# Performance work log

Hardware: AMD Instinct MI355X
Metric: run time of the kernel (lower is better)

## Reference

```python
import jax, jax.numpy as jnp
import numpy as np

H = 16
LN_EPS = 1e-5


def setup_inputs() -> dict:
    key = jax.random.key(0)
    ks = jax.random.split(key, 8)
    B, N, D = 2, 2048, 1024
    s = D ** -0.5
    return {
        "q_s": jax.random.normal(ks[0], (B, N, D), jnp.float32),
        "pos_emb": jax.random.normal(ks[1], (B, N, D), jnp.float32),
        "Wq": jax.random.normal(ks[2], (D, D), jnp.float32) * s,
        "Wk": jax.random.normal(ks[3], (D, D), jnp.float32) * s,
        "Wv": jax.random.normal(ks[4], (D, D), jnp.float32) * s,
        "Wo": jax.random.normal(ks[5], (D, D), jnp.float32) * s,
        "bo": jnp.zeros((D,), jnp.float32),
        "ln_g": jnp.ones((D,), jnp.float32),
        "ln_b": jnp.zeros((D,), jnp.float32),
    }


def _split_heads(t):
    b, n, d = t.shape
    return t.reshape(b, n, H, d // H).transpose(0, 2, 1, 3)  # b h n d


def reference(q_s, pos_emb, Wq, Wk, Wv, Wo, bo, ln_g, ln_b):
    # self-attention: k_s = v_s = q_s
    q = _split_heads(q_s @ Wq)
    k = _split_heads(q_s @ Wk)
    v = _split_heads(q_s @ Wv)
    p = _split_heads(pos_emb)
    scale = q.shape[-1] ** -0.5
    # content-content + content-position attention logits: [b,h,i,j]
    att = (jnp.einsum('bhid,bhjd->bhij', q, k) + jnp.einsum('bhid,bhjd->bhij', q, p)) * scale
    att = jax.nn.softmax(att, axis=-1)
    o = jnp.einsum('bhij,bhjd->bhid', att, v)
    b, h, n, d = o.shape
    o = o.transpose(0, 2, 1, 3).reshape(b, n, h * d)
    o = o @ Wo + bo  # out_layer (dropout rate 0 -> identity)
    x = o + q_s  # residual
    mu = jnp.mean(x, axis=-1, keepdims=True)
    var = jnp.var(x, axis=-1, keepdims=True)
    return (x - mu) * jax.lax.rsqrt(var + LN_EPS) * ln_g + ln_b
```

## Files before the change

kernel.cpp:

```cpp
#include <hip/hip_runtime.h>
#include <hip/hip_bf16.h>
#include <stdint.h>

typedef unsigned short u16;
typedef unsigned int u32;
typedef short s16x8 __attribute__((ext_vector_type(8)));
typedef short s16x4 __attribute__((ext_vector_type(4)));
typedef float f32x4 __attribute__((ext_vector_type(4)));

#define MFMA(a, b, c) __builtin_amdgcn_mfma_f32_16x16x32_bf16((a), (b), (c), 0, 0, 0)

__device__ __forceinline__ u16 f2bf_rte(float f) {
  __hip_bfloat16 h = __float2bfloat16(f);
  u16 u;
  __builtin_memcpy(&u, &h, 2);
  return u;
}

__device__ __forceinline__ void gload16(const u16* g, u16* l) {
  __builtin_amdgcn_global_load_lds((const __attribute__((address_space(1))) u32*)g,
                                   (__attribute__((address_space(3))) u32*)l, 16, 0, 0);
}

__global__ __launch_bounds__(256) void k_cvt(const float* __restrict__ in,
                                             u16* __restrict__ out, int n8) {
  int i = blockIdx.x * 256 + threadIdx.x;
  if (i >= n8) return;
  const f32x4* p = (const f32x4*)(in + (size_t)i * 8);
  f32x4 a = p[0], b = p[1];
  s16x8 o;
  for (int k = 0; k < 4; ++k) o[k] = (short)f2bf_rte(a[k]);
  for (int k = 0; k < 4; ++k) o[4 + k] = (short)f2bf_rte(b[k]);
  *(s16x8*)(out + (size_t)i * 8) = o;
}

__global__ __launch_bounds__(256) void k_transpose_w(const float* __restrict__ W0,
                                                     const float* __restrict__ W1,
                                                     const float* __restrict__ W2,
                                                     const float* __restrict__ W3,
                                                     u16* __restrict__ out) {
  const int z = blockIdx.z;
  const float* in = (z == 0) ? W0 : (z == 1) ? W1 : (z == 2) ? W2 : W3;
  u16* o = out + (size_t)z * 1024 * 1024;
  __shared__ u16 tile[64][65];
  const int t = threadIdx.x, tx = t & 63, ty = t >> 6;
  const int r0 = blockIdx.y * 64, c0 = blockIdx.x * 64;
  for (int rr = 0; rr < 16; ++rr) {
    int row = rr * 4 + ty;
    tile[row][tx] = f2bf_rte(in[(size_t)(r0 + row) * 1024 + c0 + tx]);
  }
  __syncthreads();
  for (int rr = 0; rr < 16; ++rr) {
    int row = rr * 4 + ty;
    o[(size_t)(c0 + row) * 1024 + r0 + tx] = tile[tx][row];
  }
}

__global__ __launch_bounds__(256) void k_transpose_v(const u16* __restrict__ V,
                                                     u16* __restrict__ Vt) {
  __shared__ u16 tile[64][65];
  const int t = threadIdx.x, tx = t & 63, ty = t >> 6;
  const int j0 = blockIdx.x * 64;
  const int bh = blockIdx.y;
  const u16* src = V + (size_t)bh * 2048 * 64;
  u16* dst = Vt + (size_t)bh * 64 * 2048;
  for (int rr = 0; rr < 16; ++rr) {
    int row = rr * 4 + ty;
    tile[row][tx] = src[(size_t)(j0 + row) * 64 + tx];
  }
  __syncthreads();
  for (int rr = 0; rr < 16; ++rr) {
    int d = rr * 4 + ty;
    dst[(size_t)d * 2048 + j0 + tx] = tile[tx][d];
  }
}

__global__ __launch_bounds__(256) void k_qkv_gemm(const u16* __restrict__ X,
                                                  const u16* __restrict__ WT,
                                                  const float* __restrict__ pos,
                                                  u16* __restrict__ Qh,
                                                  u16* __restrict__ Kh,
                                                  u16* __restrict__ Vh) {
  __shared__ u16 As[2][4096];
  __shared__ u16 Bs[2][4096];
  const int t = threadIdx.x;
  const int lane = t & 63, wid = t >> 6;
  const int wr = wid >> 1, wc = wid & 1;
  const int g = lane >> 4, lr = lane & 15;
  const int lin = blockIdx.y * 24 + blockIdx.x;
  const int swz = (lin & 7) * 96 + (lin >> 3);
  const int m0 = (swz / 24) * 128, n0 = (swz % 24) * 128;

  const int srcRow = t >> 2;
  const int srcKsw = ((t & 3) * 8) ^ (((t >> 3) & 3) << 3);
  const u16* aSrc = &X[(size_t)(m0 + srcRow) * 1024 + srcKsw];
  const u16* bSrc = &WT[(size_t)(n0 + srcRow) * 1024 + srcKsw];

  const int csw = (g * 8) ^ (((lr >> 1) & 3) << 3);

  f32x4 acc[4][4] = {};

#define QKV_STAGE(buf, k0)                                   \
  {                                                          \
    gload16(aSrc + (k0), &As[buf][wid * 512]);               \
    gload16(aSrc + 65536 + (k0), &As[buf][wid * 512 + 2048]);\
    gload16(bSrc + (k0), &Bs[buf][wid * 512]);               \
    gload16(bSrc + 65536 + (k0), &Bs[buf][wid * 512 + 2048]);\
  }

  QKV_STAGE(0, 0);
  int cur = 0;
  for (int k0 = 0; k0 < 1024; k0 += 32) {
    __syncthreads();
    if (k0 < 992) QKV_STAGE(cur ^ 1, k0 + 32);
    s16x8 a[4], b[4];
#pragma unroll
    for (int mi = 0; mi < 4; ++mi)
      a[mi] = *(const s16x8*)&As[cur][(wr * 64 + mi * 16 + lr) * 32 + csw];
#pragma unroll
    for (int nj = 0; nj < 4; ++nj)
      b[nj] = *(const s16x8*)&Bs[cur][(wc * 64 + nj * 16 + lr) * 32 + csw];
#pragma unroll
    for (int mi = 0; mi < 4; ++mi)
#pragma unroll
      for (int nj = 0; nj < 4; ++nj)
        acc[mi][nj] = MFMA(a[mi], b[nj], acc[mi][nj]);
    cur ^= 1;
  }
#undef QKV_STAGE

  const float QSCALE = 0.125f * 1.44269504f;
  for (int mi = 0; mi < 4; ++mi) {
    for (int nj = 0; nj < 4; ++nj) {
      const int n_g = n0 + wc * 64 + nj * 16 + lr;
      const int buf = n_g >> 10;
      const int col = n_g & 1023;
      const int h = col >> 6, d = col & 63;
      u16* dst = (buf == 0) ? Qh : ((buf == 1) ? Kh : Vh);
      for (int r = 0; r < 4; ++r) {
        const int row = m0 + wr * 64 + mi * 16 + g * 4 + r;
        const int b = row >> 11, n = row & 2047;
        float v = acc[mi][nj][r];
        if (buf == 1) v += pos[(size_t)row * 1024 + col];
        if (buf == 0) v *= QSCALE;
        dst[(size_t)((b * 16 + h) * 2048 + n) * 64 + d] = f2bf_rte(v);
      }
    }
  }
}

__global__ __launch_bounds__(512, 4) void k_attn(const u16* __restrict__ Qh,
                                                 const u16* __restrict__ Kh,
                                                 const u16* __restrict__ Vt,
                                                 u16* __restrict__ Oh) {
  const int t = threadIdx.x, lane = t & 63, wid = t >> 6;
  const int g = lane >> 4, lr = lane & 15;
  const int hid = blockIdx.x;
  const int lid = (hid & 7) * 64 + (hid >> 3);
  const int bh = lid >> 4, itile = lid & 15;
  const int i0 = itile * 128 + wid * 16;

  __shared__ char Ks[2][8192];
  __shared__ char Vs[2][8192];

  const u16* Qp = Qh + (size_t)bh * 2048 * 64;
  const u16* Kp = Kh + (size_t)bh * 2048 * 64;
  const u16* Vp = Vt + (size_t)bh * 64 * 2048;

  s16x8 aq[2];
  aq[0] = *(const s16x8*)&Qp[(size_t)(i0 + lr) * 64 + g * 8];
  aq[1] = *(const s16x8*)&Qp[(size_t)(i0 + lr) * 64 + 32 + g * 8];

  f32x4 oa[4] = {};
  float ms = -1e30f, ls = 0.f;

  const int srow = t >> 3;
  const int sch = (t & 7) * 16;
  const int swz = (srow & 7) << 4;
  const int sb = (srow * 128 + sch) ^ swz;
  const u16* kB = &Kp[(size_t)srow * 64 + (sch >> 1)];
  const u16* vB = &Vp[(size_t)srow * 2048 + (sch >> 1)];

  s16x8 kr = *(const s16x8*)kB;
  s16x8 vr = *(const s16x8*)vB;
  *(s16x8*)(Ks[0] + sb) = kr;
  *(s16x8*)(Vs[0] + sb) = vr;
  __syncthreads();

  for (int tt = 0; tt < 32; ++tt) {
    const int cur = tt & 1;
    if (tt < 31) {
      const size_t j1 = (size_t)(tt + 1) * 64;
      kr = *(const s16x8*)(kB + j1 * 64);
      vr = *(const s16x8*)(vB + j1);
    }
    const char* Kc = Ks[cur];
    const char* Vc = Vs[cur];

    f32x4 s[4] = {};
    __builtin_amdgcn_s_setprio(1);
#pragma unroll
    for (int jf = 0; jf < 4; ++jf) {
      const int row = jf * 16 + lr;
      const int bw = (row & 7) << 4;
      s16x8 bk0 = *(const s16x8*)(Kc + ((row * 128 + g * 16) ^ bw));
      s16x8 bk1 = *(const s16x8*)(Kc + ((row * 128 + 64 + g * 16) ^ bw));
      s[jf] = MFMA(bk0, aq[0], s[jf]);
      s[jf] = MFMA(bk1, aq[1], s[jf]);
    }
    __builtin_amdgcn_s_setprio(0);

    float tl = s[0][0];
#pragma unroll
    for (int jf = 0; jf < 4; ++jf)
#pragma unroll
      for (int r = 0; r < 4; ++r)
        if (jf | r) tl = fmaxf(tl, s[jf][r]);
    if (!__all(tl <= ms + 8.f)) {
      float tm = fmaxf(tl, __shfl_xor(tl, 16, 64));
      tm = fmaxf(tm, __shfl_xor(tm, 32, 64));
      float mn = fmaxf(ms, tm);
      float al = __builtin_amdgcn_exp2f(ms - mn);
      ls *= al;
      ms = mn;
#pragma unroll
      for (int r = 0; r < 4; ++r) {
        float ab = __shfl(al, g * 4 + r, 64);
#pragma unroll
        for (int df = 0; df < 4; ++df) oa[df][r] *= ab;
      }
    }

#pragma unroll
    for (int jf = 0; jf < 4; ++jf)
#pragma unroll
      for (int r = 0; r < 4; ++r) {
        float p = __builtin_amdgcn_exp2f(s[jf][r] - ms);
        s[jf][r] = p;
        ls += p;
      }

    u32 pk[4][2];
#pragma unroll
    for (int jf = 0; jf < 4; ++jf) {
      asm("v_cvt_pk_bf16_f32 %0, %1, %2" : "=v"(pk[jf][0]) : "v"(s[jf][0]), "v"(s[jf][1]));
      asm("v_cvt_pk_bf16_f32 %0, %1, %2" : "=v"(pk[jf][1]) : "v"(s[jf][2]), "v"(s[jf][3]));
    }

    s16x8 pa[2];
#pragma unroll
    for (int c = 0; c < 2; ++c) {
      u32 w_[4];
#pragma unroll
      for (int wl = 0; wl < 2; ++wl) {
        u32 A = pk[2 * c][wl], B = pk[2 * c + 1][wl];
        asm("v_permlane32_swap_b32 %0, %1" : "+v"(A), "+v"(B));
        asm("v_permlane16_swap_b32 %0, %1" : "+v"(A), "+v"(B));
        w_[wl] = A;
        w_[2 + wl] = B;
      }
      __builtin_memcpy(&pa[c], w_, 16);
    }

    __builtin_amdgcn_s_setprio(1);
#pragma unroll
    for (int df = 0; df < 4; ++df) {
      const int row = df * 16 + lr;
      const int bw = (row & 7) << 4;
      s16x8 bv0 = *(const s16x8*)(Vc + ((row * 128 + g * 16) ^ bw));
      s16x8 bv1 = *(const s16x8*)(Vc + ((row * 128 + 64 + g * 16) ^ bw));
      oa[df] = MFMA(pa[0], bv0, oa[df]);
      oa[df] = MFMA(pa[1], bv1, oa[df]);
    }
    __builtin_amdgcn_s_setprio(0);

    if (tt < 31) {
      *(s16x8*)(Ks[cur ^ 1] + sb) = kr;
      *(s16x8*)(Vs[cur ^ 1] + sb) = vr;
    }
    __syncthreads();
  }

  ls += __shfl_xor(ls, 16, 64);
  ls += __shfl_xor(ls, 32, 64);
  float lb[4];
#pragma unroll
  for (int r = 0; r < 4; ++r) lb[r] = __shfl(ls, g * 4 + r, 64);

  u16* Op = Oh + (size_t)bh * 2048 * 64;
#pragma unroll
  for (int df = 0; df < 4; ++df)
#pragma unroll
    for (int r = 0; r < 4; ++r) {
      const int row0 = i0 + g * 4 + r;
      Op[(size_t)row0 * 64 + df * 16 + lr] = f2bf_rte(oa[df][r] / lb[r]);
    }
}

__global__ __launch_bounds__(256) void k_out_gemm(const u16* __restrict__ Oh,
                                                  const u16* __restrict__ WTo,
                                                  const float* __restrict__ bo,
                                                  const float* __restrict__ qs,
                                                  float* __restrict__ X) {
  __shared__ u16 As[2][4096];
  __shared__ u16 Bs[2][4096];
  const int t = threadIdx.x;
  const int lane = t & 63, wid = t >> 6;
  const int wr = wid >> 1, wc = wid & 1;
  const int g = lane >> 4, lr = lane & 15;
  const int lin = blockIdx.y * 8 + blockIdx.x;
  const int swz = (lin & 7) * 32 + (lin >> 3);
  const int m0 = (swz / 8) * 128, n0 = (swz % 8) * 128;

  const int srcRow = t >> 2;
  const int srcKsw = ((t & 3) * 8) ^ (((t >> 3) & 3) << 3);
  const int rg = m0 + srcRow, bb0 = rg >> 11, nn0 = rg & 2047;
  const int rg2 = rg + 64, bb2 = rg2 >> 11, nn2 = rg2 & 2047;
  const u16* bSrc = &WTo[(size_t)(n0 + srcRow) * 1024 + srcKsw];
  const int csw = (g * 8) ^ (((lr >> 1) & 3) << 3);

  f32x4 acc[4][4] = {};

#define OUT_STAGE(buf, k0)                                                        \
  {                                                                               \
    const int h_ = (k0) >> 6, d_ = ((k0) & 63) + srcKsw;                          \
    gload16(&Oh[((size_t)(bb0 * 16 + h_) * 2048 + nn0) * 64 + d_],                \
            &As[buf][wid * 512]);                                                 \
    gload16(&Oh[((size_t)(bb2 * 16 + h_) * 2048 + nn2) * 64 + d_],                \
            &As[buf][wid * 512 + 2048]);                                          \
    gload16(bSrc + (k0), &Bs[buf][wid * 512]);                                    \
    gload16(bSrc + 65536 + (k0), &Bs[buf][wid * 512 + 2048]);                     \
  }

  OUT_STAGE(0, 0);
  int cur = 0;
  for (int k0 = 0; k0 < 1024; k0 += 32) {
    __syncthreads();
    if (k0 < 992) OUT_STAGE(cur ^ 1, k0 + 32);
    s16x8 a[4], b[4];
#pragma unroll
    for (int mi = 0; mi < 4; ++mi)
      a[mi] = *(const s16x8*)&As[cur][(wr * 64 + mi * 16 + lr) * 32 + csw];
#pragma unroll
    for (int nj = 0; nj < 4; ++nj)
      b[nj] = *(const s16x8*)&Bs[cur][(wc * 64 + nj * 16 + lr) * 32 + csw];
#pragma unroll
    for (int mi = 0; mi < 4; ++mi)
#pragma unroll
      for (int nj = 0; nj < 4; ++nj)
        acc[mi][nj] = MFMA(a[mi], b[nj], acc[mi][nj]);
    cur ^= 1;
  }
#undef OUT_STAGE

  for (int mi = 0; mi < 4; ++mi) {
    for (int nj = 0; nj < 4; ++nj) {
      const int col = n0 + wc * 64 + nj * 16 + lr;
      for (int r = 0; r < 4; ++r) {
        const int row = m0 + wr * 64 + mi * 16 + g * 4 + r;
        float v = acc[mi][nj][r] + bo[col] + qs[(size_t)row * 1024 + col];
        X[(size_t)row * 1024 + col] = v;
      }
    }
  }
}

__global__ __launch_bounds__(256) void k_ln(const float* __restrict__ X,
                                            const float* __restrict__ gg,
                                            const float* __restrict__ bb,
                                            float* __restrict__ out) {
  const int row = blockIdx.x, t = threadIdx.x;
  const int wid = t >> 6, lane = t & 63;
  const float* xr = X + (size_t)row * 1024;
  f32x4 x = *(const f32x4*)&xr[t * 4];
  float s1 = x[0] + x[1] + x[2] + x[3];
  float s2 = x[0] * x[0] + x[1] * x[1] + x[2] * x[2] + x[3] * x[3];
  for (int off = 32; off > 0; off >>= 1) {
    s1 += __shfl_down(s1, off, 64);
    s2 += __shfl_down(s2, off, 64);
  }
  __shared__ float red[2][4];
  if (lane == 0) { red[0][wid] = s1; red[1][wid] = s2; }
  __syncthreads();
  s1 = red[0][0] + red[0][1] + red[0][2] + red[0][3];
  s2 = red[1][0] + red[1][1] + red[1][2] + red[1][3];
  const float mu = s1 * (1.f / 1024.f);
  const float var = s2 * (1.f / 1024.f) - mu * mu;
  const float rstd = rsqrtf(var + 1e-5f);
  f32x4 gv = *(const f32x4*)&gg[t * 4];
  f32x4 bv = *(const f32x4*)&bb[t * 4];
  f32x4 ov;
  for (int i = 0; i < 4; ++i) ov[i] = (x[i] - mu) * rstd * gv[i] + bv[i];
  *(f32x4*)&out[(size_t)row * 1024 + t * 4] = ov;
}

extern "C" void kernel_launch(void* const* d_in, const int* in_sizes, int n_in,
                              void* d_out, int out_size, void* d_ws, size_t ws_size,
                              hipStream_t stream) {
  (void)in_sizes; (void)n_in; (void)out_size; (void)ws_size;
  const float* q_s = (const float*)d_in[0];
  const float* pos = (const float*)d_in[1];
  const float* Wq = (const float*)d_in[2];
  const float* Wk = (const float*)d_in[3];
  const float* Wv = (const float*)d_in[4];
  const float* Wo = (const float*)d_in[5];
  const float* bo = (const float*)d_in[6];
  const float* lng = (const float*)d_in[7];
  const float* lnb = (const float*)d_in[8];
  float* out = (float*)d_out;

  u16* ws = (u16*)d_ws;
  const size_t MB1 = 1024 * 1024;
  u16* WT  = ws;
  u16* Xbf = ws + 4 * MB1;
  u16* Qh  = Xbf + 4 * MB1;
  u16* Kh  = Qh + 4 * MB1;
  u16* Vh  = Kh + 4 * MB1;
  u16* Vt  = Vh + 4 * MB1;
  u16* Oh  = Vt + 4 * MB1;
  float* Xb = (float*)Qh;

  dim3 blk(256);
  k_cvt<<<dim3(2048), blk, 0, stream>>>(q_s, Xbf, 4 * MB1 / 8);
  k_transpose_w<<<dim3(16, 16, 4), blk, 0, stream>>>(Wq, Wk, Wv, Wo, WT);
  k_qkv_gemm<<<dim3(24, 32), blk, 0, stream>>>(Xbf, WT, pos, Qh, Kh, Vh);
  k_transpose_v<<<dim3(32, 32), blk, 0, stream>>>(Vh, Vt);
  k_attn<<<dim3(512), dim3(512), 0, stream>>>(Qh, Kh, Vt, Oh);
  k_out_gemm<<<dim3(8, 32), blk, 0, stream>>>(Oh, WT + 3 * MB1, bo, q_s, Xb);
  k_ln<<<4096, blk, 0, stream>>>(Xb, lng, lnb, out);
}
```

Before: 146.3 us.

## Triple-buffer LDS in QKV and output GEMMs with explicit vmcnt waits

Both projection GEMMs go from a double-buffered LDS pipeline to a three-stage one. Two k-tiles are prefetched ahead, and partial s_waitcnt vmcnt counts let loads stay in flight across iterations. The goal is to hide global-to-LDS latency behind MFMA work. The cost is 50% more LDS per block and two barriers per iteration. Correctness now depends on the hand-written vmcnt counts and barrier placement.

```diff
diff --git a/kernel.cpp b/kernel.cpp
--- a/kernel.cpp
+++ b/kernel.cpp
@@ -81,8 +81,8 @@
                                                   u16* __restrict__ Qh,
                                                   u16* __restrict__ Kh,
                                                   u16* __restrict__ Vh) {
-  __shared__ u16 As[2][4096];
-  __shared__ u16 Bs[2][4096];
+  __shared__ u16 As[3][4096];
+  __shared__ u16 Bs[3][4096];
   const int t = threadIdx.x;
   const int lane = t & 63, wid = t >> 6;
   const int wr = wid >> 1, wc = wid & 1;
@@ -109,10 +109,19 @@
   }
 
   QKV_STAGE(0, 0);
-  int cur = 0;
-  for (int k0 = 0; k0 < 1024; k0 += 32) {
-    __syncthreads();
-    if (k0 < 992) QKV_STAGE(cur ^ 1, k0 + 32);
+  QKV_STAGE(1, 32);
+  QKV_STAGE(2, 64);
+  for (int k = 0; k < 32; ++k) {
+    if (k < 30) {
+      asm volatile("s_waitcnt vmcnt(8)" ::: "memory");
+    } else if (k == 30) {
+      asm volatile("s_waitcnt vmcnt(4)" ::: "memory");
+    } else {
+      asm volatile("s_waitcnt vmcnt(0)" ::: "memory");
+    }
+    __builtin_amdgcn_sched_barrier(0);
+    __builtin_amdgcn_s_barrier();
+    const int cur = k % 3;
     s16x8 a[4], b[4];
 #pragma unroll
     for (int mi = 0; mi < 4; ++mi)
@@ -125,7 +134,8 @@
 #pragma unroll
       for (int nj = 0; nj < 4; ++nj)
         acc[mi][nj] = MFMA(a[mi], b[nj], acc[mi][nj]);
-    cur ^= 1;
+    __builtin_amdgcn_s_barrier();
+    if (k < 29) QKV_STAGE(cur, (k + 3) * 32);
   }
 #undef QKV_STAGE
 
@@ -302,8 +312,8 @@
                                                   const float* __restrict__ bo,
                                                   const float* __restrict__ qs,
                                                   float* __restrict__ X) {
-  __shared__ u16 As[2][4096];
-  __shared__ u16 Bs[2][4096];
+  __shared__ u16 As[3][4096];
+  __shared__ u16 Bs[3][4096];
   const int t = threadIdx.x;
   const int lane = t & 63, wid = t >> 6;
   const int wr = wid >> 1, wc = wid & 1;
@@ -333,10 +343,19 @@
   }
 
   OUT_STAGE(0, 0);
-  int cur = 0;
-  for (int k0 = 0; k0 < 1024; k0 += 32) {
-    __syncthreads();
-    if (k0 < 992) OUT_STAGE(cur ^ 1, k0 + 32);
+  OUT_STAGE(1, 32);
+  OUT_STAGE(2, 64);
+  for (int k = 0; k < 32; ++k) {
+    if (k < 30) {
+      asm volatile("s_waitcnt vmcnt(8)" ::: "memory");
+    } else if (k == 30) {
+      asm volatile("s_waitcnt vmcnt(4)" ::: "memory");
+    } else {
+      asm volatile("s_waitcnt vmcnt(0)" ::: "memory");
+    }
+    __builtin_amdgcn_sched_barrier(0);
+    __builtin_amdgcn_s_barrier();
+    const int cur = k % 3;
     s16x8 a[4], b[4];
 #pragma unroll
     for (int mi = 0; mi < 4; ++mi)
@@ -349,7 +368,8 @@
 #pragma unroll
       for (int nj = 0; nj < 4; ++nj)
         acc[mi][nj] = MFMA(a[mi], b[nj], acc[mi][nj]);
-    cur ^= 1;
+    __builtin_amdgcn_s_barrier();
+    if (k < 29) OUT_STAGE(cur, (k + 3) * 32);
   }
 #undef OUT_STAGE
 
```

New measurement: 142.9 us. 1.02x faster.
